# Performance work log

Hardware: AMD Instinct MI355X
Metric: run time of the kernel (lower is better)

## Reference

```python
import jax, jax.numpy as jnp
import numpy as np

MARGIN = 0.3
NEG_FALLBACK = 1e6  # value used when a row has no negatives


def setup_inputs() -> dict:
    key = jax.random.key(0)
    k1, k2 = jax.random.split(key)
    N, D, NUM_IDS = 8192, 256, 512
    feat = jax.random.normal(k1, (N, D), dtype=jnp.float32)
    labels = jax.random.randint(k2, (N,), 0, NUM_IDS, dtype=jnp.int64)
    return {"feat": feat, "labels": labels}


def reference(feat, labels):
    N = feat.shape[0]
    sq_norms = jnp.sum(feat * feat, axis=1)  # [N]
    sq = sq_norms[:, None] + sq_norms[None, :] - 2.0 * (feat @ feat.T)  # [N,N]
    sq = jnp.maximum(sq, 0.0)
    # safe sqrt (zero distance on the diagonal would otherwise give nan grads)
    dist = jnp.where(sq > 0, jnp.sqrt(jnp.where(sq > 0, sq, 1.0)), 0.0)

    same = labels[:, None] == labels[None, :]          # [N,N] bool
    eye = jnp.eye(N, dtype=bool)
    is_pos = same & ~eye                                # exclude self-pair
    is_neg = ~same

    # hard mining: per-row masked max over positives / min over negatives
    dist_ap = jnp.where(is_pos.any(axis=1),
                        jnp.where(is_pos, dist, -jnp.inf).max(axis=1), 0.0)
    dist_an = jnp.where(is_neg.any(axis=1),
                        jnp.where(is_neg, dist, jnp.inf).min(axis=1), NEG_FALLBACK)

    # MarginRankingLoss with y=1: mean(relu(margin - (dist_an - dist_ap)))
    return jnp.mean(jnp.maximum(0.0, MARGIN + dist_ap - dist_an))
```

## Files before the change

kernel.cpp:

```cpp
#include <hip/hip_runtime.h>


constexpr int N = 8192;
constexpr int D = 256;
constexpr float MARGIN = 0.3f;
constexpr float NEG_FALLBACK = 1e6f;
constexpr float TBIG = 1e30f;

typedef __attribute__((ext_vector_type(8))) __bf16 bf16x8;
typedef __attribute__((ext_vector_type(4))) float f32x4;

__device__ __forceinline__ unsigned enc_f(float f) {
  unsigned u = __float_as_uint(f);
  return (u >> 31) ? ~u : (u | 0x80000000u);
}
__device__ __forceinline__ float dec_f(unsigned e) {
  unsigned u = (e >> 31) ? (e ^ 0x80000000u) : ~e;
  return __uint_as_float(u);
}
__device__ __forceinline__ unsigned short f2bf_rtn(float x) {
  unsigned u = __float_as_uint(x);
  return (unsigned short)((u + 0x7fffu + ((u >> 16) & 1u)) >> 16);
}


__global__ void tl_sortk(const int* __restrict__ labels, int* __restrict__ perm,
                         int* __restrict__ labp, int* __restrict__ offg) {
  __shared__ int hist[512], scan[512];
  const int tid = threadIdx.x;
  hist[tid] = 0;
  __syncthreads();
  for (int i = tid; i < N; i += 512) atomicAdd(&hist[labels[i]], 1);
  __syncthreads();
  const int v = hist[tid];
  scan[tid] = v;
  __syncthreads();
#pragma unroll
  for (int d = 1; d < 512; d <<= 1) {
    int t = (tid >= d) ? scan[tid - d] : 0;
    __syncthreads();
    scan[tid] += t;
    __syncthreads();
  }
  const int excl = scan[tid] - v;
  offg[tid] = excl;
  if (tid == 511) offg[512] = scan[511];
  hist[tid] = excl;
  __syncthreads();
  for (int i = tid; i < N; i += 512) {
    const int L = labels[i];
    const int pos = atomicAdd(&hist[L], 1);
    perm[pos] = i;
    labp[pos] = L;
  }
}


__global__ void tl_pass0p(const float* __restrict__ feat, const int* __restrict__ perm,
                          float* __restrict__ norms, unsigned* __restrict__ ap,
                          unsigned* __restrict__ an, unsigned short* __restrict__ P,
                          float* __restrict__ out) {
  const int p = blockIdx.x * 4 + (threadIdx.x >> 6);
  const int lane = threadIdx.x & 63;
  const int src = perm[p];
  float4 f = reinterpret_cast<const float4*>(feat + (size_t)src * D)[lane];
  ushort4 h;
  h.x = f2bf_rtn(f.x); h.y = f2bf_rtn(f.y); h.z = f2bf_rtn(f.z); h.w = f2bf_rtn(f.w);
  reinterpret_cast<ushort4*>(P + (size_t)p * D)[lane] = h;
  float s = fmaf(f.x, f.x, fmaf(f.y, f.y, fmaf(f.z, f.z, f.w * f.w)));
#pragma unroll
  for (int off = 32; off > 0; off >>= 1) s += __shfl_down(s, off, 64);
  if (lane == 0) {
    norms[p] = s;
    ap[p] = enc_f(-TBIG);
    an[p] = enc_f(TBIG);
  }
  if (p == 0 && lane == 0) out[0] = 0.0f;
}


__global__ __launch_bounds__(256, 2)
void tl_pass1s(const unsigned short* __restrict__ P, const int* __restrict__ labp,
               const float* __restrict__ norms, const int* __restrict__ offg,
               unsigned* __restrict__ ap, unsigned* __restrict__ an) {
  __shared__ unsigned short lB[2][128][128];

  const int tid = threadIdx.x;
  const int wave = tid >> 6;
  const int lane = tid & 63;
  const int c = lane & 15;
  const int q = lane >> 4;
  const int i0 = blockIdx.y * 128;
  const int j0 = blockIdx.x * 1024;
  const int wrow = i0 + wave * 32;

  const int lo = offg[labp[i0]];
  const int hi = offg[labp[i0 + 127] + 1];

  bf16x8 af[2][8];
#pragma unroll
  for (int a = 0; a < 2; ++a)
#pragma unroll
    for (int t2 = 0; t2 < 8; ++t2)
      af[a][t2] = *(const bf16x8*)(P + (size_t)(wrow + a * 16 + c) * D + t2 * 32 + q * 8);

  f32x4 acc[2][8];
#pragma unroll
  for (int a = 0; a < 2; ++a)
#pragma unroll
    for (int b = 0; b < 8; ++b) acc[a][b] = (f32x4){0.f, 0.f, 0.f, 0.f};

  float vp[2][4], vn[2][4];
#pragma unroll
  for (int a = 0; a < 2; ++a)
#pragma unroll
    for (int r = 0; r < 4; ++r) { vp[a][r] = -TBIG; vn[a][r] = TBIG; }

  const int rsub = lane >> 4;
  const int g15 = lane & 15;

#define STAGE(BUF, S1)                                                                  \
  do {                                                                                  \
    const int jt_ = (S1) >> 1;                                                          \
    const int kc_ = ((S1) & 1) * 128;                                                   \
    const int jb_ = j0 + jt_ * 128;                                                     \
    _Pragma("unroll") for (int t = 0; t < 8; ++t) {                                     \
      const int rA_ = wave * 32 + t * 4;                                                \
      const int sg_ = g15 ^ rsub ^ ((t & 1) * 4);                                       \
      const unsigned short* gp_ = P + (size_t)(jb_ + rA_ + rsub) * D + kc_ + sg_ * 8;   \
      __builtin_amdgcn_global_load_lds(                                                 \
          (const __attribute__((address_space(1))) void*)gp_,                           \
          (__attribute__((address_space(3))) void*)&lB[BUF][rA_][0], 16, 0, 0);         \
    }                                                                                   \
  } while (0)

#define CHALF(KB)                                                                       \
  do {                                                                                  \
    _Pragma("unroll") for (int ks = 0; ks < 4; ++ks) {                                  \
      const int gsel_ = ((ks * 4 + q) ^ (c & 7)) * 8;                                   \
      bf16x8 bfr[8];                                                                    \
      _Pragma("unroll") for (int b = 0; b < 8; ++b)                                     \
          bfr[b] = *(const bf16x8*)&lB[cur][b * 16 + c][gsel_];                         \
      _Pragma("unroll") for (int a = 0; a < 2; ++a)                                     \
          _Pragma("unroll") for (int b = 0; b < 8; ++b)                                 \
              acc[a][b] = __builtin_amdgcn_mfma_f32_16x16x32_bf16(                      \
                  af[a][(KB) + ks], bfr[b], acc[a][b], 0, 0, 0);                        \
    }                                                                                   \
  } while (0)

  STAGE(0, 0);
  __syncthreads();
  int cur = 0;

#pragma unroll 2
  for (int s = 0; s < 16; ++s) {
    if (s < 15) STAGE(cur ^ 1, s + 1);
    if ((s & 1) == 0) CHALF(0); else CHALF(4);

    if (s & 1) {
      const int jt = s >> 1;
      const int jb0 = j0 + jt * 128;
      const bool careful = (jb0 < hi) && (jb0 + 128 > lo);
      if (!careful) {
#pragma unroll
        for (int b = 0; b < 8; ++b) {
          const float njb = norms[jb0 + b * 16 + c];
#pragma unroll
          for (int a = 0; a < 2; ++a)
#pragma unroll
            for (int r = 0; r < 4; ++r)
              vn[a][r] = fminf(vn[a][r], fmaf(-2.f, acc[a][b][r], njb));
        }
      } else {
        int lj[8], cj[8];
        float nj[8];
#pragma unroll
        for (int b = 0; b < 8; ++b) {
          cj[b] = jb0 + b * 16 + c;
          nj[b] = norms[cj[b]];
          lj[b] = labp[cj[b]];
        }
#pragma unroll
        for (int a = 0; a < 2; ++a)
#pragma unroll
          for (int r = 0; r < 4; ++r) {
            const int rg = wrow + a * 16 + q * 4 + r;
            const int li = labp[rg];
            float vpl = vp[a][r], vnl = vn[a][r];
#pragma unroll
            for (int b = 0; b < 8; ++b) {
              const float t = fmaf(-2.f, acc[a][b][r], nj[b]);
              const bool sm = (lj[b] == li);
              const bool dg = (cj[b] == rg);
              vpl = fmaxf(vpl, (sm && !dg) ? t : -TBIG);
              vnl = fminf(vnl, sm ? TBIG : t);
            }
            vp[a][r] = vpl;
            vn[a][r] = vnl;
          }
      }
#pragma unroll
      for (int a = 0; a < 2; ++a)
#pragma unroll
        for (int b = 0; b < 8; ++b) acc[a][b] = (f32x4){0.f, 0.f, 0.f, 0.f};
    }
    __syncthreads();
    cur ^= 1;
  }
#undef STAGE
#undef CHALF

#pragma unroll
  for (int a = 0; a < 2; ++a)
#pragma unroll
    for (int r = 0; r < 4; ++r) {
      float p = vp[a][r], n = vn[a][r];
#pragma unroll
      for (int m = 1; m < 16; m <<= 1) {
        p = fmaxf(p, __shfl_xor(p, m, 64));
        n = fminf(n, __shfl_xor(n, m, 64));
      }
      if (c == 0) {
        const int rg = wrow + a * 16 + q * 4 + r;
        atomicMax(&ap[rg], enc_f(p));
        atomicMin(&an[rg], enc_f(n));
      }
    }
}


__global__ void tl_pass2f(const unsigned* __restrict__ ap, const unsigned* __restrict__ an,
                          const float* __restrict__ norms, float* __restrict__ out) {
  int r = blockIdx.x * 256 + threadIdx.x;
  float ni = norms[r];
  float tpv = dec_f(ap[r]);
  float tnv = dec_f(an[r]);
  float dap = (tpv < -1e29f) ? 0.f : sqrtf(fmaxf(ni + tpv, 0.f));
  float dan = (tnv > 1e29f) ? NEG_FALLBACK : sqrtf(fmaxf(ni + tnv, 0.f));
  float v = fmaxf(0.f, MARGIN + dap - dan) * (1.0f / (float)N);
#pragma unroll
  for (int off = 32; off > 0; off >>= 1) v += __shfl_down(v, off, 64);
  __shared__ float red[4];
  int lane = threadIdx.x & 63, w = threadIdx.x >> 6;
  if (lane == 0) red[w] = v;
  __syncthreads();
  if (threadIdx.x == 0) atomicAdd(out, red[0] + red[1] + red[2] + red[3]);
}


constexpr int FB_BK = 32;
constexpr int FB_JSPLIT = 8;
constexpr int FB_JRANGE = N / FB_JSPLIT;
constexpr int FB_LDS = 132;

__global__ void tl_pass0_fb(const float* __restrict__ feat, float* __restrict__ norms,
                            float* __restrict__ ap, float* __restrict__ an,
                            float* __restrict__ out) {
  int row = blockIdx.x * 4 + (threadIdx.x >> 6);
  int lane = threadIdx.x & 63;
  float4 f = reinterpret_cast<const float4*>(feat + (size_t)row * D)[lane];
  float s = f.x * f.x + f.y * f.y + f.z * f.z + f.w * f.w;
#pragma unroll
  for (int off = 32; off > 0; off >>= 1) s += __shfl_down(s, off, 64);
  if (lane == 0) { norms[row] = s; ap[row] = 0.0f; an[row] = NEG_FALLBACK; }
  if (row == 0 && lane == 0) out[0] = 0.0f;
}

__global__ __launch_bounds__(256, 2)
void tl_pass1_fb(const float* __restrict__ feat, const int* __restrict__ labels,
                 const float* __restrict__ norms,
                 unsigned int* __restrict__ ap, unsigned int* __restrict__ an) {
  __shared__ float As[FB_BK][FB_LDS];
  __shared__ float Bs[FB_BK][FB_LDS];
  const int tid = threadIdx.x;
  const int tx = tid & 15, ty = tid >> 4;
  const int ib0 = blockIdx.y * 128;
  const int jbase = blockIdx.x * FB_JRANGE;
  float ni[8]; int li[8]; int ri[8];
#pragma unroll
  for (int a = 0; a < 8; ++a) {
    int r = ty * 4 + (a & 3) + ((a >> 2) << 6);
    ri[a] = ib0 + r; ni[a] = norms[ri[a]]; li[a] = labels[ri[a]];
  }
  float apv[8], anv[8];
#pragma unroll
  for (int a = 0; a < 8; ++a) { apv[a] = 0.0f; anv[a] = NEG_FALLBACK; }
  for (int jt = 0; jt < FB_JRANGE; jt += 128) {
    const int jb = jbase + jt;
    float acc[8][8];
#pragma unroll
    for (int a = 0; a < 8; ++a)
#pragma unroll
      for (int b = 0; b < 8; ++b) acc[a][b] = 0.0f;
    for (int kc = 0; kc < D; kc += FB_BK) {
#pragma unroll
      for (int u = 0; u < 4; ++u) {
        int lin = tid + u * 256;
        int row = lin >> 3, c4 = lin & 7;
        float4 va = *reinterpret_cast<const float4*>(feat + (size_t)(ib0 + row) * D + kc + c4 * 4);
        As[c4 * 4 + 0][row] = va.x; As[c4 * 4 + 1][row] = va.y;
        As[c4 * 4 + 2][row] = va.z; As[c4 * 4 + 3][row] = va.w;
        float4 vb = *reinterpret_cast<const float4*>(feat + (size_t)(jb + row) * D + kc + c4 * 4);
        Bs[c4 * 4 + 0][row] = vb.x; Bs[c4 * 4 + 1][row] = vb.y;
        Bs[c4 * 4 + 2][row] = vb.z; Bs[c4 * 4 + 3][row] = vb.w;
      }
      __syncthreads();
#pragma unroll 8
      for (int k = 0; k < FB_BK; ++k) {
        float4 a0 = *reinterpret_cast<const float4*>(&As[k][ty * 4]);
        float4 a1 = *reinterpret_cast<const float4*>(&As[k][64 + ty * 4]);
        float4 b0 = *reinterpret_cast<const float4*>(&Bs[k][tx * 4]);
        float4 b1 = *reinterpret_cast<const float4*>(&Bs[k][64 + tx * 4]);
        float av[8] = {a0.x, a0.y, a0.z, a0.w, a1.x, a1.y, a1.z, a1.w};
        float bv[8] = {b0.x, b0.y, b0.z, b0.w, b1.x, b1.y, b1.z, b1.w};
#pragma unroll
        for (int a = 0; a < 8; ++a)
#pragma unroll
          for (int b = 0; b < 8; ++b) acc[a][b] = fmaf(av[a], bv[b], acc[a][b]);
      }
      __syncthreads();
    }
#pragma unroll
    for (int b = 0; b < 8; ++b) {
      int cjx = jb + tx * 4 + (b & 3) + ((b >> 2) << 6);
      float njx = norms[cjx]; int ljx = labels[cjx];
#pragma unroll
      for (int a = 0; a < 8; ++a) {
        float sq = fmaxf(ni[a] + njx - 2.0f * acc[a][b], 0.0f);
        float dist = sqrtf(sq);
        if (li[a] == ljx) { if (ri[a] != cjx) apv[a] = fmaxf(apv[a], dist); }
        else anv[a] = fminf(anv[a], dist);
      }
    }
  }
  __syncthreads();
  float* red = &As[0][0];
#pragma unroll
  for (int a = 0; a < 8; ++a) {
    int r = ty * 4 + (a & 3) + ((a >> 2) << 6);
    red[r * 16 + tx] = apv[a];
  }
  __syncthreads();
  if (tid < 128) {
    float m = red[tid * 16];
#pragma unroll
    for (int t = 1; t < 16; ++t) m = fmaxf(m, red[tid * 16 + t]);
    atomicMax(&ap[ib0 + tid], __float_as_uint(m));
  }
  __syncthreads();
#pragma unroll
  for (int a = 0; a < 8; ++a) {
    int r = ty * 4 + (a & 3) + ((a >> 2) << 6);
    red[r * 16 + tx] = anv[a];
  }
  __syncthreads();
  if (tid < 128) {
    float m = red[tid * 16];
#pragma unroll
    for (int t = 1; t < 16; ++t) m = fminf(m, red[tid * 16 + t]);
    atomicMin(&an[ib0 + tid], __float_as_uint(m));
  }
}

__global__ void tl_pass2_fb(const float* __restrict__ ap, const float* __restrict__ an,
                            float* __restrict__ out) {
  int r = blockIdx.x * 256 + threadIdx.x;
  float v = fmaxf(0.0f, MARGIN + ap[r] - an[r]) * (1.0f / (float)N);
#pragma unroll
  for (int off = 32; off > 0; off >>= 1) v += __shfl_down(v, off, 64);
  __shared__ float red[4];
  int lane = threadIdx.x & 63, w = threadIdx.x >> 6;
  if (lane == 0) red[w] = v;
  __syncthreads();
  if (threadIdx.x == 0) atomicAdd(out, red[0] + red[1] + red[2] + red[3]);
}


extern "C" void kernel_launch(void* const* d_in, const int* in_sizes, int n_in,
                              void* d_out, int out_size, void* d_ws, size_t ws_size,
                              hipStream_t stream) {
  const float* feat = (const float*)d_in[0];
  const int* labels = (const int*)d_in[1];
  float* out = (float*)d_out;

  float* norms = (float*)d_ws;
  unsigned* ap = (unsigned*)(norms + N);
  unsigned* an = ap + N;
  int* perm = (int*)(an + N);
  int* labp = perm + N;
  int* offg = labp + N;
  unsigned short* P = (unsigned short*)(offg + 520);
  const size_t NEED = (size_t)5 * N * 4 + 520 * 4 + (size_t)N * D * 2;

  if (ws_size >= NEED) {
    tl_sortk<<<1, 512, 0, stream>>>(labels, perm, labp, offg);
    tl_pass0p<<<N / 4, 256, 0, stream>>>(feat, perm, norms, ap, an, P, out);
    dim3 grid1(8, N / 128);
    tl_pass1s<<<grid1, 256, 0, stream>>>(P, labp, norms, offg, ap, an);
    tl_pass2f<<<N / 256, 256, 0, stream>>>(ap, an, norms, out);
  } else {
    float* apf = (float*)ap;
    float* anf = (float*)an;
    tl_pass0_fb<<<N / 4, 256, 0, stream>>>(feat, norms, apf, anf, out);
    dim3 grid1(FB_JSPLIT, N / 128);
    tl_pass1_fb<<<grid1, 256, 0, stream>>>(feat, labels, norms, (unsigned*)apf, (unsigned*)anf);
    tl_pass2_fb<<<N / 256, 256, 0, stream>>>(apf, anf, out);
  }
}
```

Baseline: 116.7 us.

## Halve LDS tile and j-span for higher occupancy; parallelize label sort with wave scans

The main distance kernel now stages 64-wide K chunks instead of 128 (halving shared memory), covers 512 columns per block instead of 1024, doubles the grid in x, and raises launch bounds to 4 blocks per CU so more waves can hide memory latency. The pipeline is restructured as a fully unrolled 4x4 loop with a sync per stage, which adds more barriers and more atomics in the final row reduction. The label counting sort now runs with 1024 threads, holds labels in registers, and replaces the shared-memory Hillis-Steele scan with wave shuffle scans plus a small per-wave base, cutting barrier count in that single-block kernel.

Result: slower. 167.4 us (+43.5%).

```diff
diff --git a/kernel.cpp b/kernel.cpp
--- a/kernel.cpp
+++ b/kernel.cpp
@@ -24,34 +24,54 @@
 }
 
 
-__global__ void tl_sortk(const int* __restrict__ labels, int* __restrict__ perm,
-                         int* __restrict__ labp, int* __restrict__ offg) {
-  __shared__ int hist[512], scan[512];
+__global__ __launch_bounds__(1024)
+void tl_sortk(const int* __restrict__ labels, int* __restrict__ perm,
+              int* __restrict__ labp, int* __restrict__ offg) {
+  __shared__ int hist[512];
+  __shared__ int wsum[8];
+  __shared__ int wbase[8];
   const int tid = threadIdx.x;
-  hist[tid] = 0;
-  __syncthreads();
-  for (int i = tid; i < N; i += 512) atomicAdd(&hist[labels[i]], 1);
-  __syncthreads();
-  const int v = hist[tid];
-  scan[tid] = v;
-  __syncthreads();
-#pragma unroll
-  for (int d = 1; d < 512; d <<= 1) {
-    int t = (tid >= d) ? scan[tid - d] : 0;
-    __syncthreads();
-    scan[tid] += t;
-    __syncthreads();
-  }
-  const int excl = scan[tid] - v;
-  offg[tid] = excl;
-  if (tid == 511) offg[512] = scan[511];
-  hist[tid] = excl;
-  __syncthreads();
-  for (int i = tid; i < N; i += 512) {
-    const int L = labels[i];
-    const int pos = atomicAdd(&hist[L], 1);
-    perm[pos] = i;
-    labp[pos] = L;
+  const int lane = tid & 63;
+  const int w = tid >> 6;
+  if (tid < 512) hist[tid] = 0;
+  __syncthreads();
+  int l8[8];
+#pragma unroll
+  for (int k = 0; k < 8; ++k) {
+    l8[k] = labels[tid + k * 1024];
+    atomicAdd(&hist[l8[k]], 1);
+  }
+  __syncthreads();
+  int v = 0, sc = 0;
+  if (tid < 512) {
+    v = hist[tid];
+    sc = v;
+#pragma unroll
+    for (int d = 1; d < 64; d <<= 1) {
+      int t = __shfl_up(sc, d, 64);
+      if (lane >= d) sc += t;
+    }
+    if (lane == 63) wsum[w] = sc;
+  }
+  __syncthreads();
+  if (tid == 0) {
+    int a = 0;
+#pragma unroll
+    for (int i = 0; i < 8; ++i) { wbase[i] = a; a += wsum[i]; }
+  }
+  __syncthreads();
+  if (tid < 512) {
+    const int excl = wbase[w] + sc - v;
+    offg[tid] = excl;
+    hist[tid] = excl;
+  }
+  if (tid == 0) offg[512] = N;
+  __syncthreads();
+#pragma unroll
+  for (int k = 0; k < 8; ++k) {
+    const int pos = atomicAdd(&hist[l8[k]], 1);
+    perm[pos] = tid + k * 1024;
+    labp[pos] = l8[k];
   }
 }
 
@@ -79,11 +99,11 @@
 }
 
 
-__global__ __launch_bounds__(256, 2)
+__global__ __launch_bounds__(256, 4)
 void tl_pass1s(const unsigned short* __restrict__ P, const int* __restrict__ labp,
                const float* __restrict__ norms, const int* __restrict__ offg,
                unsigned* __restrict__ ap, unsigned* __restrict__ an) {
-  __shared__ unsigned short lB[2][128][128];
+  __shared__ unsigned short lB[2][128][64];
 
   const int tid = threadIdx.x;
   const int wave = tid >> 6;
@@ -91,7 +111,7 @@
   const int c = lane & 15;
   const int q = lane >> 4;
   const int i0 = blockIdx.y * 128;
-  const int j0 = blockIdx.x * 1024;
+  const int j0 = blockIdx.x * 512;
   const int wrow = i0 + wave * 32;
 
   const int lo = offg[labp[i0]];
@@ -116,99 +136,100 @@
 #pragma unroll
     for (int r = 0; r < 4; ++r) { vp[a][r] = -TBIG; vn[a][r] = TBIG; }
 
-  const int rsub = lane >> 4;
-  const int g15 = lane & 15;
-
-#define STAGE(BUF, S1)                                                                  \
+  const int rsub = lane >> 3;
+  const int g7 = lane & 7;
+
+#define STAGE(S1)                                                                       \
   do {                                                                                  \
-    const int jt_ = (S1) >> 1;                                                          \
-    const int kc_ = ((S1) & 1) * 128;                                                   \
+    const int jt_ = (S1) >> 2;                                                          \
+    const int kc_ = ((S1) & 3) * 64;                                                    \
     const int jb_ = j0 + jt_ * 128;                                                     \
-    _Pragma("unroll") for (int t = 0; t < 8; ++t) {                                     \
-      const int rA_ = wave * 32 + t * 4;                                                \
-      const int sg_ = g15 ^ rsub ^ ((t & 1) * 4);                                       \
+    const int buf_ = (S1) & 1;                                                          \
+    _Pragma("unroll") for (int t = 0; t < 4; ++t) {                                     \
+      const int rA_ = wave * 32 + t * 8;                                                \
+      const int sg_ = g7 ^ rsub;                                                        \
       const unsigned short* gp_ = P + (size_t)(jb_ + rA_ + rsub) * D + kc_ + sg_ * 8;   \
       __builtin_amdgcn_global_load_lds(                                                 \
           (const __attribute__((address_space(1))) void*)gp_,                           \
-          (__attribute__((address_space(3))) void*)&lB[BUF][rA_][0], 16, 0, 0);         \
+          (__attribute__((address_space(3))) void*)&lB[buf_][rA_][0], 16, 0, 0);        \
     }                                                                                   \
   } while (0)
 
-#define CHALF(KB)                                                                       \
-  do {                                                                                  \
-    _Pragma("unroll") for (int ks = 0; ks < 4; ++ks) {                                  \
-      const int gsel_ = ((ks * 4 + q) ^ (c & 7)) * 8;                                   \
-      bf16x8 bfr[8];                                                                    \
-      _Pragma("unroll") for (int b = 0; b < 8; ++b)                                     \
-          bfr[b] = *(const bf16x8*)&lB[cur][b * 16 + c][gsel_];                         \
-      _Pragma("unroll") for (int a = 0; a < 2; ++a)                                     \
-          _Pragma("unroll") for (int b = 0; b < 8; ++b)                                 \
-              acc[a][b] = __builtin_amdgcn_mfma_f32_16x16x32_bf16(                      \
-                  af[a][(KB) + ks], bfr[b], acc[a][b], 0, 0, 0);                        \
-    }                                                                                   \
-  } while (0)
-
-  STAGE(0, 0);
-  __syncthreads();
-  int cur = 0;
-
-#pragma unroll 2
-  for (int s = 0; s < 16; ++s) {
-    if (s < 15) STAGE(cur ^ 1, s + 1);
-    if ((s & 1) == 0) CHALF(0); else CHALF(4);
-
-    if (s & 1) {
-      const int jt = s >> 1;
-      const int jb0 = j0 + jt * 128;
-      const bool careful = (jb0 < hi) && (jb0 + 128 > lo);
-      if (!careful) {
-#pragma unroll
-        for (int b = 0; b < 8; ++b) {
-          const float njb = norms[jb0 + b * 16 + c];
+  STAGE(0);
+  __syncthreads();
+
+#pragma unroll
+  for (int jt = 0; jt < 4; ++jt) {
+#pragma unroll
+    for (int kk = 0; kk < 4; ++kk) {
+      const int s = jt * 4 + kk;
+      if (s < 15) STAGE(s + 1);
+
+#pragma unroll
+      for (int ks = 0; ks < 2; ++ks) {
+        const int gsel = ((ks * 4 + q) ^ (c & 7)) * 8;
+        bf16x8 bfr[8];
+#pragma unroll
+        for (int b = 0; b < 8; ++b)
+          bfr[b] = *(const bf16x8*)&lB[s & 1][b * 16 + c][gsel];
+#pragma unroll
+        for (int a = 0; a < 2; ++a)
+#pragma unroll
+          for (int b = 0; b < 8; ++b)
+            acc[a][b] = __builtin_amdgcn_mfma_f32_16x16x32_bf16(
+                af[a][kk * 2 + ks], bfr[b], acc[a][b], 0, 0, 0);
+      }
+
+      if (kk == 3) {
+        const int jb0 = j0 + jt * 128;
+        const bool careful = (jb0 < hi) && (jb0 + 128 > lo);
+        if (!careful) {
+#pragma unroll
+          for (int b = 0; b < 8; ++b) {
+            const float njb = norms[jb0 + b * 16 + c];
+#pragma unroll
+            for (int a = 0; a < 2; ++a)
+#pragma unroll
+              for (int r = 0; r < 4; ++r)
+                vn[a][r] = fminf(vn[a][r], fmaf(-2.f, acc[a][b][r], njb));
+          }
+        } else {
+          int lj[8], cj[8];
+          float nj[8];
+#pragma unroll
+          for (int b = 0; b < 8; ++b) {
+            cj[b] = jb0 + b * 16 + c;
+            nj[b] = norms[cj[b]];
+            lj[b] = labp[cj[b]];
+          }
 #pragma unroll
           for (int a = 0; a < 2; ++a)
 #pragma unroll
-            for (int r = 0; r < 4; ++r)
-              vn[a][r] = fminf(vn[a][r], fmaf(-2.f, acc[a][b][r], njb));
+            for (int r = 0; r < 4; ++r) {
+              const int rg = wrow + a * 16 + q * 4 + r;
+              const int li = labp[rg];
+              float vpl = vp[a][r], vnl = vn[a][r];
+#pragma unroll
+              for (int b = 0; b < 8; ++b) {
+                const float t = fmaf(-2.f, acc[a][b][r], nj[b]);
+                const bool sm = (lj[b] == li);
+                const bool dg = (cj[b] == rg);
+                vpl = fmaxf(vpl, (sm && !dg) ? t : -TBIG);
+                vnl = fminf(vnl, sm ? TBIG : t);
+              }
+              vp[a][r] = vpl;
+              vn[a][r] = vnl;
+            }
         }
-      } else {
-        int lj[8], cj[8];
-        float nj[8];
-#pragma unroll
-        for (int b = 0; b < 8; ++b) {
-          cj[b] = jb0 + b * 16 + c;
-          nj[b] = norms[cj[b]];
-          lj[b] = labp[cj[b]];
-        }
 #pragma unroll
         for (int a = 0; a < 2; ++a)
 #pragma unroll
-          for (int r = 0; r < 4; ++r) {
-            const int rg = wrow + a * 16 + q * 4 + r;
-            const int li = labp[rg];
-            float vpl = vp[a][r], vnl = vn[a][r];
-#pragma unroll
-            for (int b = 0; b < 8; ++b) {
-              const float t = fmaf(-2.f, acc[a][b][r], nj[b]);
-              const bool sm = (lj[b] == li);
-              const bool dg = (cj[b] == rg);
-              vpl = fmaxf(vpl, (sm && !dg) ? t : -TBIG);
-              vnl = fminf(vnl, sm ? TBIG : t);
-            }
-            vp[a][r] = vpl;
-            vn[a][r] = vnl;
-          }
-      }
-#pragma unroll
-      for (int a = 0; a < 2; ++a)
-#pragma unroll
-        for (int b = 0; b < 8; ++b) acc[a][b] = (f32x4){0.f, 0.f, 0.f, 0.f};
+          for (int b = 0; b < 8; ++b) acc[a][b] = (f32x4){0.f, 0.f, 0.f, 0.f};
+      }
+      __syncthreads();
     }
-    __syncthreads();
-    cur ^= 1;
   }
 #undef STAGE
-#undef CHALF
 
 #pragma unroll
   for (int a = 0; a < 2; ++a)
@@ -393,9 +414,9 @@
   const size_t NEED = (size_t)5 * N * 4 + 520 * 4 + (size_t)N * D * 2;
 
   if (ws_size >= NEED) {
-    tl_sortk<<<1, 512, 0, stream>>>(labels, perm, labp, offg);
+    tl_sortk<<<1, 1024, 0, stream>>>(labels, perm, labp, offg);
     tl_pass0p<<<N / 4, 256, 0, stream>>>(feat, perm, norms, ap, an, P, out);
-    dim3 grid1(8, N / 128);
+    dim3 grid1(16, N / 128);
     tl_pass1s<<<grid1, 256, 0, stream>>>(P, labp, norms, offg, ap, an);
     tl_pass2f<<<N / 256, 256, 0, stream>>>(ap, an, norms, out);
   } else {
```
